# Kernel tuning notes

Hardware: AMD Instinct MI355X
Metric: run time of the kernel (lower is better)

Reference implementation:

```python
import jax, jax.numpy as jnp
import numpy as np
from jax.scipy.special import logsumexp

B, T, F = 32, 256, 32   # batch, line width (time), line height (features)
HID = 128
VOCAB = 100             # blank index = VOCAB
LBL = 32                # label length
NEG = -1e30


def _mdlstm(x, Wx, Wh1, Wh2, b):
    # x: [B, H, W, C] -> 2D LSTM: outer scan over width, inner scan over height
    Bb, H, W, C = x.shape
    hid = Wh1.shape[0]

    def col_step(carry, x_col):
        c_left, h_left = carry  # [H, B, hid] states from previous column

        def row_step(rc, inp):
            c_up, h_up = rc          # [B, hid] from previous row
            x_ij, c_l, h_l = inp     # [B, C], [B, hid], [B, hid]
            z = x_ij @ Wx + h_l @ Wh1 + h_up @ Wh2 + b  # [B, 5*hid]
            i_, g_, f1, f2, o_ = jnp.split(z, 5, axis=-1)
            c = jax.nn.sigmoid(f1) * c_l + jax.nn.sigmoid(f2) * c_up + jax.nn.sigmoid(i_) * jnp.tanh(g_)
            h = jax.nn.sigmoid(o_) * jnp.tanh(c)
            return (c, h), (c, h)

        z0 = jnp.zeros((Bb, hid), x.dtype)
        _, (c_col, h_col) = jax.lax.scan(row_step, (z0, z0), (x_col, c_left, h_left))
        return (c_col, h_col), h_col

    x_t = jnp.transpose(x, (2, 1, 0, 3))  # [W, H, B, C]
    zc = jnp.zeros((H, Bb, hid), x.dtype)
    _, hs = jax.lax.scan(col_step, (zc, zc), x_t)  # [W, H, B, hid]
    return jnp.transpose(hs, (2, 1, 0, 3))  # [B, H, W, hid]


def _ctc_loss(logp, labels, blank):
    # logp: [B, T, V] log-softmax; labels: [B, L] int in [0, blank)
    Bb, Tt, V = logp.shape
    Ll = labels.shape[1]
    S = 2 * Ll + 1
    ext = jnp.full((Bb, S), blank, dtype=labels.dtype).at[:, 1::2].set(labels)  # blank-interleaved
    lp_ext = jnp.take_along_axis(logp, jnp.broadcast_to(ext[:, None, :], (Bb, Tt, S)), axis=2)  # [B,T,S]
    prev2 = jnp.concatenate([jnp.full((Bb, 2), blank, dtype=ext.dtype), ext[:, :-2]], axis=1)
    skip = (ext != blank) & (ext != prev2)
    skip = skip.at[:, :2].set(False)
    alpha0 = jnp.full((Bb, S), NEG, logp.dtype).at[:, 0].set(lp_ext[:, 0, 0]).at[:, 1].set(lp_ext[:, 0, 1])

    def step(alpha, lp_t):
        a1 = jnp.concatenate([jnp.full((Bb, 1), NEG, alpha.dtype), alpha[:, :-1]], axis=1)
        a2 = jnp.concatenate([jnp.full((Bb, 2), NEG, alpha.dtype), alpha[:, :-2]], axis=1)
        a2 = jnp.where(skip, a2, NEG)
        new = logsumexp(jnp.stack([alpha, a1, a2], axis=0), axis=0) + lp_t
        return new, None

    alphaT, _ = jax.lax.scan(step, alpha0, jnp.transpose(lp_ext, (1, 0, 2))[1:])
    ll = logsumexp(jnp.stack([alphaT[:, -1], alphaT[:, -2]], axis=0), axis=0)
    return -ll  # [B]


def setup_inputs() -> dict:
    key = jax.random.key(0)
    ks = jax.random.split(key, 8)
    s = 0.08
    return {
        "X": jax.random.normal(ks[0], (B, T, F), jnp.float32),
        "y": jax.random.randint(ks[1], (B, LBL), 0, VOCAB),
        "Wx": jax.random.normal(ks[2], (1, 5 * HID), jnp.float32) * s,
        "Wh1": jax.random.normal(ks[3], (HID, 5 * HID), jnp.float32) * s,
        "Wh2": jax.random.normal(ks[4], (HID, 5 * HID), jnp.float32) * s,
        "b": jax.random.normal(ks[5], (5 * HID,), jnp.float32) * 0.01,
        "W_fc": jax.random.normal(ks[6], (HID, VOCAB + 1), jnp.float32) * s,
        "b_fc": jax.random.normal(ks[7], (VOCAB + 1,), jnp.float32) * 0.01,
    }


def reference(X, y, Wx, Wh1, Wh2, b, W_fc, b_fc):
    x = jnp.transpose(X, (0, 2, 1))[..., None]        # [B, F, T, 1] (image)
    h = _mdlstm(x, Wx, Wh1, Wh2, b)                    # [B, F, T, HID]
    feat = jnp.sum(h, axis=1)                          # collapse over height -> [B, T, HID]
    logits = feat @ W_fc + b_fc                        # [B, T, VOCAB+1]
    logp = jax.nn.log_softmax(logits, axis=-1)
    return _ctc_loss(logp, y, VOCAB)                   # per-example CTC loss [B]
```

## Files before the change

### kernel.cpp

```cpp
#include <hip/hip_runtime.h>

#define NEGF (-1e30f)

typedef __attribute__((ext_vector_type(8))) short short8;
typedef __attribute__((ext_vector_type(4))) float float4v;

template <bool V> struct BC { static constexpr bool value = V; };

__device__ __forceinline__ short f2bf(float f) {
  union { float f; unsigned u; } v; v.f = f;
  unsigned r = v.u + 0x7fffu + ((v.u >> 16) & 1u);
  return (short)(r >> 16);
}
__device__ __forceinline__ float fastrcp(float x) { return __builtin_amdgcn_rcpf(x); }
__device__ __forceinline__ float clamp15(float x) { return fminf(15.0f, fmaxf(-15.0f, x)); }

__global__ void prep_w_kernel(const float* __restrict__ Wh1, const float* __restrict__ Wh2,
                              short* __restrict__ wsW) {
  int t = blockIdx.x * 256 + threadIdx.x;
  int lane = t & 63;
  int frag = t >> 6;
  int nt = frag >> 3, kk = frag & 7;
  int n  = nt * 16 + (lane & 15);
  int kb = kk * 32 + (lane >> 4) * 8;
  short8 v;
#pragma unroll
  for (int j = 0; j < 8; ++j) {
    int k = kb + j;
    float w = (k < 128) ? Wh1[k * 640 + n] : Wh2[(k - 128) * 640 + n];
    v[j] = f2bf(w);
  }
  ((short8*)wsW)[frag * 64 + lane] = v;
}

__global__ __launch_bounds__(512)
void mdlstm_kernel(const float* __restrict__ X, const short* __restrict__ wsW,
                   const float* __restrict__ Wx, const float* __restrict__ bias,
                   float* __restrict__ feat, float* __restrict__ bH0,
                   float* __restrict__ bC0, int* __restrict__ flagA,
                   int* __restrict__ flagB) {
  __shared__ __align__(16) short h_buf[2][17][136];
  __shared__ __align__(16) short wlds[128 * 512];
  __shared__ __align__(16) short wlds2[16 * 512];

  const int blk  = blockIdx.x;
  const int bat  = blk >> 1;
  const bool isB = blk & 1;
  const int tid  = threadIdx.x;
  const int lane = tid & 63;
  const int g    = tid >> 6;
  const int col  = lane & 15;
  const int quad = lane >> 4;
  const int jj   = g * 16 + col;

  for (int i = tid; i < 2 * 17 * 136 / 2; i += 512) ((int*)h_buf)[i] = 0;
  {
    const uint4* src = (const uint4*)(wsW + 192 * 512);
    uint4* dst = (uint4*)wlds;
    for (int i = tid; i < 8192; i += 512) dst[i] = src[i];
    const uint4* s4 = (const uint4*)wsW;
    uint4* d2 = (uint4*)wlds2;
    for (int i = tid; i < 1024; i += 512) {
      int f = i >> 6, off = i & 63;
      int srcf = 128 + 8 * (f >> 1) + (f & 1);
      d2[i] = s4[srcf * 64 + off];
    }
  }

  float wx[5], bg[5];
#pragma unroll
  for (int q = 0; q < 5; ++q) {
    wx[q] = Wx[q * 128 + jj];
    bg[q] = bias[q * 128 + jj];
  }
  float cp[4] = {0.f, 0.f, 0.f, 0.f};
  float c15 = 0.0f;

  const float* Xg = X + bat * 8192;
  float* fb = feat + bat * 32768;
  float* bH = bH0 + bat * 32 * 128;
  float* bC = bC0 + bat * 32 * 128;
  int* fA = flagA + bat;
  int* fB = flagB + bat;
  const short8* W8 = (const short8*)wsW;
  const short8* pW0 = W8 + ((0 * 8 + g) * 8) * 64 + lane;
  const short8* pW1 = W8 + ((1 * 8 + g) * 8) * 64 + lane;
  const short8* pW2 = W8 + ((2 * 8 + g) * 8) * 64 + lane;
  const short8* pL3 = (const short8*)&wlds[((0 * 8 + g) * 8) * 512 + lane * 8];
  const short8* pL4 = (const short8*)&wlds[((1 * 8 + g) * 8) * 512 + lane * 8];
  const short8* pL2 = (const short8*)&wlds2[(g * 2) * 512 + lane * 8];
  const int mbase = (isB ? 16 : 0) + quad * 4;
  const int widx0 = (isB ? 1 : 0) + quad * 4;
  const float* pX = Xg - 31 * mbase;
  float* pF = fb + jj - 128 * mbase;
  __syncthreads();

  auto step = [&](int d, auto isb_, auto allv_) {
    constexpr bool IsB = decltype(isb_)::value;
    constexpr bool ALLV = decltype(allv_)::value;
    const int rbuf = (d + 1) & 1, wbuf = d & 1;
    float4v acc[5];
#pragma unroll
    for (int q = 0; q < 5; ++q) acc[q] = (float4v){bg[q], bg[q], bg[q], bg[q]};
    const short8 z8 = (short8){0, 0, 0, 0, 0, 0, 0, 0};
#pragma unroll
    for (int kk = 0; kk < 8; ++kk) {
      const int up = (kk >= 4) ? 1 : 0;
      const int cc = (kk & 3) * 32 + quad * 8;
      int row = col + (IsB ? 1 : 0) - up;
      short8 a0 = (IsB || row >= 0) ? *(const short8*)&h_buf[rbuf][row][cc] : z8;
      short8 b3 = pL3[kk * 64];
      acc[3] = __builtin_amdgcn_mfma_f32_16x16x32_bf16(a0, b3, acc[3], 0, 0, 0);
      short8 b4 = pL4[kk * 64];
      acc[4] = __builtin_amdgcn_mfma_f32_16x16x32_bf16(a0, b4, acc[4], 0, 0, 0);
      short8 b2 = (kk < 2) ? pL2[kk * 64] : pW2[kk * 64];
      acc[2] = __builtin_amdgcn_mfma_f32_16x16x32_bf16(a0, b2, acc[2], 0, 0, 0);
      short8 b0 = pW0[kk * 64];
      acc[0] = __builtin_amdgcn_mfma_f32_16x16x32_bf16(a0, b0, acc[0], 0, 0, 0);
      short8 b1 = pW1[kk * 64];
      acc[1] = __builtin_amdgcn_mfma_f32_16x16x32_bf16(a0, b1, acc[1], 0, 0, 0);
    }

    float t0 = __shfl_up(cp[3], 16);
    float cu[4];
    cu[0] = quad ? t0 : (IsB ? c15 : 0.0f);
    cu[1] = cp[0]; cu[2] = cp[1]; cu[3] = cp[2];
    const float* pXd = pX + d * 32;
    float* pFd = pF + d * 128;
    float xm[4];
#pragma unroll
    for (int r = 0; r < 4; ++r) {
      int w = d - (mbase + r);
      if (ALLV || (w >= 0 && w < 256)) xm[r] = pXd[-31 * r];
    }
#pragma unroll
    for (int r = 0; r < 4; ++r) {
      const int w = d - (mbase + r);
      if (ALLV || (w >= 0 && w < 256)) {
        float c_up = cu[r];
        float c_l  = cp[r];
        float x    = xm[r];
        float zi = clamp15(fmaf(x, wx[0], acc[0][r]));
        float zg = clamp15(fmaf(x, wx[1], acc[1][r]));
        float z1 = clamp15(fmaf(x, wx[2], acc[2][r]));
        float z2 = clamp15(fmaf(x, wx[3], acc[3][r]));
        float zo = clamp15(fmaf(x, wx[4], acc[4][r]));
        float e1 = __expf(z1), e2 = __expf(z2), ei = __expf(zi), eg = __expf(2.0f * zg);
        float A1 = 1.0f + e1, A2 = 1.0f + e2, Ai = 1.0f + ei, G = 1.0f + eg;
        float P = Ai * G, Q = A1 * A2;
        float rD = fastrcp(P * Q);
        float c = (e1 * c_l * (A2 * P) + e2 * c_up * (A1 * P) + ei * (eg - 1.0f) * Q) * rD;
        float eo = __expf(-zo);
        float ec = __expf(2.0f * clamp15(c));
        float h = (ec - 1.0f) * fastrcp((1.0f + eo) * (ec + 1.0f));
        cp[r] = c;
        h_buf[wbuf][widx0 + r][jj] = f2bf(h);
        atomicAdd(&pFd[-128 * r], h);
        if (!IsB && r == 3 && quad == 3 && d >= 15) {
          const int slot = (d & 31) * 128 + jj;
          atomicExch(&bH[slot], h);
          atomicExch(&bC[slot], c);
        }
      }
    }
  };

  auto receive = [&](int e) {
    if (e <= 271) {
      if (lane == 0) { while (atomicAdd(fA, 0) < e) {} }
      const int slot = ((e - 1) & 31) * 128 + jj;
      if (quad == 1) {
        float hv = atomicAdd(&bH[slot], 0.0f);
        h_buf[(e + 1) & 1][0][jj] = f2bf(hv);
      } else if (quad == 0) {
        c15 = atomicAdd(&bC[slot], 0.0f);
      }
    } else {
      if (quad == 1) h_buf[(e + 1) & 1][0][jj] = 0;
      else if (quad == 0) c15 = 0.0f;
    }
  };

  BC<true> T; BC<false> F;
  if (!isB) {
    for (int d = 0; d < 15; ++d)   { step(d, F, F); __syncthreads(); }
    for (int d = 15; d < 256; ++d) {
      if (d >= 47 && lane == 0) { while (atomicAdd(fB, 0) < d - 32) {} }
      step(d, F, T); __syncthreads();
      if (tid == 0) atomicExch(fA, d + 1);
    }
    for (int d = 256; d < 271; ++d) {
      if (lane == 0) { while (atomicAdd(fB, 0) < d - 32) {} }
      step(d, F, F); __syncthreads();
      if (tid == 0) atomicExch(fA, d + 1);
    }
  } else {
    receive(16);
    for (int d = 16; d < 31; ++d)  { __syncthreads(); step(d, T, F); receive(d + 1); if (tid == 0) atomicExch(fB, d); }
    for (int d = 31; d < 272; ++d) { __syncthreads(); step(d, T, T); receive(d + 1); if (tid == 0) atomicExch(fB, d); }
    for (int d = 272; d < 287; ++d){ __syncthreads(); step(d, T, F); if (d < 286) receive(d + 1); if (tid == 0) atomicExch(fB, d); }
  }
}

__global__ __launch_bounds__(256)
void logits_kernel(const float* __restrict__ feat, const float* __restrict__ Wfc,
                   const float* __restrict__ bfc, float* __restrict__ logp) {
  __shared__ float sW[128 * 101];
  __shared__ float sF[8][128];
  __shared__ float sL[8][104];
  __shared__ float sLse[8];
  const int tid = threadIdx.x;
  const int b  = blockIdx.x >> 5;
  const int t0 = (blockIdx.x & 31) * 8;

  for (int i = tid; i < 128 * 101; i += 256) sW[i] = Wfc[i];
  for (int i = tid; i < 8 * 128; i += 256)
    sF[i >> 7][i & 127] = feat[(b * 256 + t0 + (i >> 7)) * 128 + (i & 127)];
  __syncthreads();
  for (int idx = tid; idx < 8 * 101; idx += 256) {
    int tr = idx / 101, v = idx - tr * 101;
    float s = bfc[v];
#pragma unroll 4
    for (int k = 0; k < 128; ++k) s += sF[tr][k] * sW[k * 101 + v];
    sL[tr][v] = s;
  }
  __syncthreads();
  if (tid < 8) {
    float m = NEGF;
    for (int v = 0; v < 101; ++v) m = fmaxf(m, sL[tid][v]);
    float su = 0.0f;
    for (int v = 0; v < 101; ++v) su += __expf(sL[tid][v] - m);
    sLse[tid] = m + __logf(su);
  }
  __syncthreads();
  for (int idx = tid; idx < 8 * 101; idx += 256) {
    int tr = idx / 101, v = idx - tr * 101;
    logp[(b * 256 + t0 + tr) * 101 + v] = sL[tr][v] - sLse[tr];
  }
}

__global__ __launch_bounds__(64)
void ctc_kernel(const float* __restrict__ logp, const int* __restrict__ y,
                float* __restrict__ out) {
  const int b = blockIdx.x;
  const int l = threadIdx.x;
  const float* lpb = logp + b * 256 * 101;
  const int* yb = y + b * 32;
  int lab = (l & 1) ? yb[l >> 1] : 100;
  bool skip = (l & 1) && (l >= 3) && (yb[l >> 1] != yb[(l >> 1) - 1]);

  float a   = (l == 0) ? lpb[100] : ((l == 1) ? lpb[lab] : NEGF);
  float a64 = NEGF;
  float pl[4], pb[4];
#pragma unroll
  for (int tt = 0; tt < 4; ++tt) {
    pl[tt] = lpb[(1 + tt) * 101 + lab];
    pb[tt] = lpb[(1 + tt) * 101 + 100];
  }
#pragma unroll 4
  for (int t = 1; t < 256; ++t) {
    const int s = (t - 1) & 3;
    float lpl = pl[s], lpbk = pb[s];
    if (t + 4 < 256) {
      pl[s] = lpb[(t + 4) * 101 + lab];
      pb[s] = lpb[(t + 4) * 101 + 100];
    }
    float am1 = __shfl_up(a, 1); if (l == 0) am1 = NEGF;
    float am2 = __shfl_up(a, 2); if (l < 2 || !skip) am2 = NEGF;
    float m3 = fmaxf(a, fmaxf(am1, am2));
    float na = m3 + __logf(__expf(a - m3) + __expf(am1 - m3) + __expf(am2 - m3)) + lpl;
    float m2 = fmaxf(a64, a);
    float na64 = m2 + __logf(__expf(a64 - m2) + __expf(a - m2)) + lpbk;
    a = na;
    a64 = na64;
  }
  float A63 = __shfl(a, 63);
  float A64 = __shfl(a64, 63);
  if (l == 0) {
    float m = fmaxf(A63, A64);
    out[b] = -(m + __logf(__expf(A63 - m) + __expf(A64 - m)));
  }
}

extern "C" void kernel_launch(void* const* d_in, const int* in_sizes, int n_in,
                              void* d_out, int out_size, void* d_ws, size_t ws_size,
                              hipStream_t stream) {
  const float* X   = (const float*)d_in[0];
  const int*   y   = (const int*)d_in[1];
  const float* Wx  = (const float*)d_in[2];
  const float* Wh1 = (const float*)d_in[3];
  const float* Wh2 = (const float*)d_in[4];
  const float* bi  = (const float*)d_in[5];
  const float* Wfc = (const float*)d_in[6];
  const float* bfc = (const float*)d_in[7];
  float* out = (float*)d_out;

  char* ws = (char*)d_ws;
  short* wsW  = (short*)(ws);
  float* bndH = (float*)(ws + 0x50000);
  float* bndC = (float*)(ws + 0xD0000);
  int*   flgA = (int*)(ws + 0x150000);
  int*   flgB = (int*)(ws + 0x150800);
  float* logp = (float*)(ws + 0x50000);
  float* feat = (float*)(ws + 0x378000);

  hipMemsetAsync(feat, 0, 32 * 256 * 128 * sizeof(float), stream);
  prep_w_kernel<<<80, 256, 0, stream>>>(Wh1, Wh2, wsW);
  mdlstm_kernel<<<64, 512, 0, stream>>>(X, wsW, Wx, bi, feat, bndH, bndC, flgA, flgB);
  logits_kernel<<<1024, 256, 0, stream>>>(feat, Wfc, bfc, logp);
  ctc_kernel<<<32, 64, 0, stream>>>(logp, y, out);
}
```

Baseline: 877.2 us.

## Merge two-block split MDLSTM into one block per batch with register-held weights

Each batch element previously ran on two cooperating blocks that traded boundary h/c state through global memory with spin-wait flags. Now a single 512-thread block handles all 32 rows, running two MFMA row-halves per wavefront step and passing the row-16 cell state by warp shuffle. Gate weights for three gates sit in registers and the other two in LDS. Per-column feature sums build up in an LDS ring buffer instead of global atomics. This removes the cross-block flag handshakes and atomic traffic, but doubles per-block MFMA work each diagonal, halves the block count, and raises register pressure.

```diff
diff --git a/kernel.cpp b/kernel.cpp
--- a/kernel.cpp
+++ b/kernel.cpp
@@ -36,16 +36,12 @@
 __global__ __launch_bounds__(512)
 void mdlstm_kernel(const float* __restrict__ X, const short* __restrict__ wsW,
                    const float* __restrict__ Wx, const float* __restrict__ bias,
-                   float* __restrict__ feat, float* __restrict__ bH0,
-                   float* __restrict__ bC0, int* __restrict__ flagA,
-                   int* __restrict__ flagB) {
-  __shared__ __align__(16) short h_buf[2][17][136];
-  __shared__ __align__(16) short wlds[128 * 512];
-  __shared__ __align__(16) short wlds2[16 * 512];
-
-  const int blk  = blockIdx.x;
-  const int bat  = blk >> 1;
-  const bool isB = blk & 1;
+                   float* __restrict__ feat) {
+  __shared__ __align__(16) short h_buf[2][33][136];
+  __shared__ __align__(16) short wlds[14 * 4096];
+  __shared__ float featbuf[33][132];
+
+  const int bat  = blockIdx.x;
   const int tid  = threadIdx.x;
   const int lane = tid & 63;
   const int g    = tid >> 6;
@@ -53,17 +49,17 @@
   const int quad = lane >> 4;
   const int jj   = g * 16 + col;
 
-  for (int i = tid; i < 2 * 17 * 136 / 2; i += 512) ((int*)h_buf)[i] = 0;
+  for (int i = tid; i < 4488; i += 512) ((int*)h_buf)[i] = 0;
+  for (int i = tid; i < 33 * 132; i += 512) ((float*)featbuf)[i] = 0.0f;
   {
-    const uint4* src = (const uint4*)(wsW + 192 * 512);
-    uint4* dst = (uint4*)wlds;
-    for (int i = tid; i < 8192; i += 512) dst[i] = src[i];
     const uint4* s4 = (const uint4*)wsW;
-    uint4* d2 = (uint4*)wlds2;
-    for (int i = tid; i < 1024; i += 512) {
-      int f = i >> 6, off = i & 63;
-      int srcf = 128 + 8 * (f >> 1) + (f & 1);
-      d2[i] = s4[srcf * 64 + off];
+    uint4* d4 = (uint4*)wlds;
+    for (int i = tid; i < 14 * 512; i += 512) {
+      int c = i >> 9, off = i & 511;
+      int gg = off >> 6, ln = off & 63;
+      int q  = (c < 7) ? 3 : 4;
+      int kk = (c < 7) ? c : (c - 7);
+      d4[i] = s4[(((q * 8 + gg) * 8) + kk) * 64 + ln];
     }
   }
 
@@ -73,133 +69,115 @@
     wx[q] = Wx[q * 128 + jj];
     bg[q] = bias[q * 128 + jj];
   }
-  float cp[4] = {0.f, 0.f, 0.f, 0.f};
-  float c15 = 0.0f;
-
-  const float* Xg = X + bat * 8192;
+
+  const short8* W8 = (const short8*)wsW;
+  short8 rb0[8], rb1[8], rb2[8];
+#pragma unroll
+  for (int kk = 0; kk < 8; ++kk) {
+    rb0[kk] = W8[((0 * 8 + g) * 8 + kk) * 64 + lane];
+    rb1[kk] = W8[((1 * 8 + g) * 8 + kk) * 64 + lane];
+    rb2[kk] = W8[((2 * 8 + g) * 8 + kk) * 64 + lane];
+  }
+  const short8 rb37 = W8[((3 * 8 + g) * 8 + 7) * 64 + lane];
+  const short8 rb47 = W8[((4 * 8 + g) * 8 + 7) * 64 + lane];
+
+  const short8* pL3 = (const short8*)wlds + g * 64 + lane;
+  const short8* pL4 = (const short8*)wlds + 7 * 512 + g * 64 + lane;
+
+  float cp0[4] = {0.f, 0.f, 0.f, 0.f};
+  float cp1[4] = {0.f, 0.f, 0.f, 0.f};
+  const float* Xb = X + bat * 8192;
   float* fb = feat + bat * 32768;
-  float* bH = bH0 + bat * 32 * 128;
-  float* bC = bC0 + bat * 32 * 128;
-  int* fA = flagA + bat;
-  int* fB = flagB + bat;
-  const short8* W8 = (const short8*)wsW;
-  const short8* pW0 = W8 + ((0 * 8 + g) * 8) * 64 + lane;
-  const short8* pW1 = W8 + ((1 * 8 + g) * 8) * 64 + lane;
-  const short8* pW2 = W8 + ((2 * 8 + g) * 8) * 64 + lane;
-  const short8* pL3 = (const short8*)&wlds[((0 * 8 + g) * 8) * 512 + lane * 8];
-  const short8* pL4 = (const short8*)&wlds[((1 * 8 + g) * 8) * 512 + lane * 8];
-  const short8* pL2 = (const short8*)&wlds2[(g * 2) * 512 + lane * 8];
-  const int mbase = (isB ? 16 : 0) + quad * 4;
-  const int widx0 = (isB ? 1 : 0) + quad * 4;
-  const float* pX = Xg - 31 * mbase;
-  float* pF = fb + jj - 128 * mbase;
-  __syncthreads();
-
-  auto step = [&](int d, auto isb_, auto allv_) {
-    constexpr bool IsB = decltype(isb_)::value;
+
+  int sb = 0;
+  __syncthreads();
+
+  auto stepT = [&](int d, auto allv_) {
     constexpr bool ALLV = decltype(allv_)::value;
     const int rbuf = (d + 1) & 1, wbuf = d & 1;
-    float4v acc[5];
-#pragma unroll
-    for (int q = 0; q < 5; ++q) acc[q] = (float4v){bg[q], bg[q], bg[q], bg[q]};
-    const short8 z8 = (short8){0, 0, 0, 0, 0, 0, 0, 0};
+
+    if (d >= 32 && tid < 128) {
+      int fs = sb + 1; if (fs >= 33) fs = 0;
+      float v = featbuf[fs][tid];
+      featbuf[fs][tid] = 0.0f;
+      fb[(d - 32) * 128 + tid] = v;
+    }
+
+    float4v acc0[5], acc1[5];
+#pragma unroll
+    for (int q = 0; q < 5; ++q) {
+      acc0[q] = (float4v){bg[q], bg[q], bg[q], bg[q]};
+      acc1[q] = acc0[q];
+    }
 #pragma unroll
     for (int kk = 0; kk < 8; ++kk) {
-      const int up = (kk >= 4) ? 1 : 0;
-      const int cc = (kk & 3) * 32 + quad * 8;
-      int row = col + (IsB ? 1 : 0) - up;
-      short8 a0 = (IsB || row >= 0) ? *(const short8*)&h_buf[rbuf][row][cc] : z8;
-      short8 b3 = pL3[kk * 64];
-      acc[3] = __builtin_amdgcn_mfma_f32_16x16x32_bf16(a0, b3, acc[3], 0, 0, 0);
-      short8 b4 = pL4[kk * 64];
-      acc[4] = __builtin_amdgcn_mfma_f32_16x16x32_bf16(a0, b4, acc[4], 0, 0, 0);
-      short8 b2 = (kk < 2) ? pL2[kk * 64] : pW2[kk * 64];
-      acc[2] = __builtin_amdgcn_mfma_f32_16x16x32_bf16(a0, b2, acc[2], 0, 0, 0);
-      short8 b0 = pW0[kk * 64];
-      acc[0] = __builtin_amdgcn_mfma_f32_16x16x32_bf16(a0, b0, acc[0], 0, 0, 0);
-      short8 b1 = pW1[kk * 64];
-      acc[1] = __builtin_amdgcn_mfma_f32_16x16x32_bf16(a0, b1, acc[1], 0, 0, 0);
-    }
-
-    float t0 = __shfl_up(cp[3], 16);
-    float cu[4];
-    cu[0] = quad ? t0 : (IsB ? c15 : 0.0f);
-    cu[1] = cp[0]; cu[2] = cp[1]; cu[3] = cp[2];
-    const float* pXd = pX + d * 32;
-    float* pFd = pF + d * 128;
-    float xm[4];
-#pragma unroll
-    for (int r = 0; r < 4; ++r) {
-      int w = d - (mbase + r);
-      if (ALLV || (w >= 0 && w < 256)) xm[r] = pXd[-31 * r];
-    }
-#pragma unroll
-    for (int r = 0; r < 4; ++r) {
-      const int w = d - (mbase + r);
-      if (ALLV || (w >= 0 && w < 256)) {
-        float c_up = cu[r];
-        float c_l  = cp[r];
-        float x    = xm[r];
-        float zi = clamp15(fmaf(x, wx[0], acc[0][r]));
-        float zg = clamp15(fmaf(x, wx[1], acc[1][r]));
-        float z1 = clamp15(fmaf(x, wx[2], acc[2][r]));
-        float z2 = clamp15(fmaf(x, wx[3], acc[3][r]));
-        float zo = clamp15(fmaf(x, wx[4], acc[4][r]));
-        float e1 = __expf(z1), e2 = __expf(z2), ei = __expf(zi), eg = __expf(2.0f * zg);
-        float A1 = 1.0f + e1, A2 = 1.0f + e2, Ai = 1.0f + ei, G = 1.0f + eg;
-        float P = Ai * G, Q = A1 * A2;
-        float rD = fastrcp(P * Q);
-        float c = (e1 * c_l * (A2 * P) + e2 * c_up * (A1 * P) + ei * (eg - 1.0f) * Q) * rD;
-        float eo = __expf(-zo);
-        float ec = __expf(2.0f * clamp15(c));
-        float h = (ec - 1.0f) * fastrcp((1.0f + eo) * (ec + 1.0f));
-        cp[r] = c;
-        h_buf[wbuf][widx0 + r][jj] = f2bf(h);
-        atomicAdd(&pFd[-128 * r], h);
-        if (!IsB && r == 3 && quad == 3 && d >= 15) {
-          const int slot = (d & 31) * 128 + jj;
-          atomicExch(&bH[slot], h);
-          atomicExch(&bC[slot], c);
+      const int up = kk >> 2;
+      const int ccc = (kk & 3) * 32 + quad * 8;
+      short8 a0 = *(const short8*)&h_buf[rbuf][col + 1 - up][ccc];
+      short8 a1 = *(const short8*)&h_buf[rbuf][17 + col - up][ccc];
+      short8 b3 = (kk < 7) ? pL3[kk * 512] : rb37;
+      acc0[3] = __builtin_amdgcn_mfma_f32_16x16x32_bf16(a0, b3, acc0[3], 0, 0, 0);
+      acc1[3] = __builtin_amdgcn_mfma_f32_16x16x32_bf16(a1, b3, acc1[3], 0, 0, 0);
+      short8 b4 = (kk < 7) ? pL4[kk * 512] : rb47;
+      acc0[4] = __builtin_amdgcn_mfma_f32_16x16x32_bf16(a0, b4, acc0[4], 0, 0, 0);
+      acc1[4] = __builtin_amdgcn_mfma_f32_16x16x32_bf16(a1, b4, acc1[4], 0, 0, 0);
+      short8 b0 = rb0[kk];
+      acc0[0] = __builtin_amdgcn_mfma_f32_16x16x32_bf16(a0, b0, acc0[0], 0, 0, 0);
+      acc1[0] = __builtin_amdgcn_mfma_f32_16x16x32_bf16(a1, b0, acc1[0], 0, 0, 0);
+      short8 b1 = rb1[kk];
+      acc0[1] = __builtin_amdgcn_mfma_f32_16x16x32_bf16(a0, b1, acc0[1], 0, 0, 0);
+      acc1[1] = __builtin_amdgcn_mfma_f32_16x16x32_bf16(a1, b1, acc1[1], 0, 0, 0);
+      short8 b2 = rb2[kk];
+      acc0[2] = __builtin_amdgcn_mfma_f32_16x16x32_bf16(a0, b2, acc0[2], 0, 0, 0);
+      acc1[2] = __builtin_amdgcn_mfma_f32_16x16x32_bf16(a1, b2, acc1[2], 0, 0, 0);
+    }
+
+    float t00 = __shfl_up(cp0[3], 16);
+    float t10 = __shfl_up(cp1[3], 16);
+    float c15 = __shfl(cp0[3], 48 + col);
+    float cu0[4], cu1[4];
+    cu0[0] = quad ? t00 : 0.0f; cu0[1] = cp0[0]; cu0[2] = cp0[1]; cu0[3] = cp0[2];
+    cu1[0] = quad ? t10 : c15;  cu1[1] = cp1[0]; cu1[2] = cp1[1]; cu1[3] = cp1[2];
+
+    auto halfc = [&](float4v (&acc)[5], float (&cp)[4], float (&cu)[4], int mbase) {
+#pragma unroll
+      for (int r = 0; r < 4; ++r) {
+        const int m = mbase + r;
+        const int w = d - m;
+        if (ALLV || (unsigned)w < 256u) {
+          const float x = Xb[w * 32 + m];
+          float zi = clamp15(fmaf(x, wx[0], acc[0][r]));
+          float zg = clamp15(fmaf(x, wx[1], acc[1][r]));
+          float z1 = clamp15(fmaf(x, wx[2], acc[2][r]));
+          float z2 = clamp15(fmaf(x, wx[3], acc[3][r]));
+          float zo = clamp15(fmaf(x, wx[4], acc[4][r]));
+          float e1 = __expf(z1), e2 = __expf(z2), ei = __expf(zi), eg = __expf(2.0f * zg);
+          float A1 = 1.0f + e1, A2 = 1.0f + e2, Ai = 1.0f + ei, G = 1.0f + eg;
+          float P = Ai * G, Q = A1 * A2;
+          float rD = fastrcp(P * Q);
+          float c = (e1 * cp[r] * (A2 * P) + e2 * cu[r] * (A1 * P) + ei * (eg - 1.0f) * Q) * rD;
+          float eo = __expf(-zo);
+          float ec = __expf(2.0f * clamp15(c));
+          float h = (ec - 1.0f) * fastrcp((1.0f + eo) * (ec + 1.0f));
+          cp[r] = c;
+          h_buf[wbuf][1 + m][jj] = f2bf(h);
+          int s = sb - m; if (s < 0) s += 33;
+          featbuf[s][jj] += h;
         }
       }
-    }
+    };
+    halfc(acc0, cp0, cu0, quad * 4);
+    halfc(acc1, cp1, cu1, 16 + quad * 4);
+    __syncthreads();
   };
 
-  auto receive = [&](int e) {
-    if (e <= 271) {
-      if (lane == 0) { while (atomicAdd(fA, 0) < e) {} }
-      const int slot = ((e - 1) & 31) * 128 + jj;
-      if (quad == 1) {
-        float hv = atomicAdd(&bH[slot], 0.0f);
-        h_buf[(e + 1) & 1][0][jj] = f2bf(hv);
-      } else if (quad == 0) {
-        c15 = atomicAdd(&bC[slot], 0.0f);
-      }
-    } else {
-      if (quad == 1) h_buf[(e + 1) & 1][0][jj] = 0;
-      else if (quad == 0) c15 = 0.0f;
-    }
-  };
-
-  BC<true> T; BC<false> F;
-  if (!isB) {
-    for (int d = 0; d < 15; ++d)   { step(d, F, F); __syncthreads(); }
-    for (int d = 15; d < 256; ++d) {
-      if (d >= 47 && lane == 0) { while (atomicAdd(fB, 0) < d - 32) {} }
-      step(d, F, T); __syncthreads();
-      if (tid == 0) atomicExch(fA, d + 1);
-    }
-    for (int d = 256; d < 271; ++d) {
-      if (lane == 0) { while (atomicAdd(fB, 0) < d - 32) {} }
-      step(d, F, F); __syncthreads();
-      if (tid == 0) atomicExch(fA, d + 1);
-    }
-  } else {
-    receive(16);
-    for (int d = 16; d < 31; ++d)  { __syncthreads(); step(d, T, F); receive(d + 1); if (tid == 0) atomicExch(fB, d); }
-    for (int d = 31; d < 272; ++d) { __syncthreads(); step(d, T, T); receive(d + 1); if (tid == 0) atomicExch(fB, d); }
-    for (int d = 272; d < 287; ++d){ __syncthreads(); step(d, T, F); if (d < 286) receive(d + 1); if (tid == 0) atomicExch(fB, d); }
-  }
+  BC<true> Tv; BC<false> Fv;
+  for (int d = 0; d < 31; ++d)    { stepT(d, Fv); sb = (sb == 32) ? 0 : sb + 1; }
+  for (int d = 31; d < 256; ++d)  { stepT(d, Tv); sb = (sb == 32) ? 0 : sb + 1; }
+  for (int d = 256; d < 287; ++d) { stepT(d, Fv); sb = (sb == 32) ? 0 : sb + 1; }
+
+  int fs = sb + 1; if (fs >= 33) fs = 0;
+  if (tid < 128) fb[255 * 128 + tid] = featbuf[fs][tid];
 }
 
 __global__ __launch_bounds__(256)
@@ -297,16 +275,12 @@
 
   char* ws = (char*)d_ws;
   short* wsW  = (short*)(ws);
-  float* bndH = (float*)(ws + 0x50000);
-  float* bndC = (float*)(ws + 0xD0000);
-  int*   flgA = (int*)(ws + 0x150000);
-  int*   flgB = (int*)(ws + 0x150800);
   float* logp = (float*)(ws + 0x50000);
   float* feat = (float*)(ws + 0x378000);
 
   hipMemsetAsync(feat, 0, 32 * 256 * 128 * sizeof(float), stream);
   prep_w_kernel<<<80, 256, 0, stream>>>(Wh1, Wh2, wsW);
-  mdlstm_kernel<<<64, 512, 0, stream>>>(X, wsW, Wx, bi, feat, bndH, bndC, flgA, flgB);
+  mdlstm_kernel<<<32, 512, 0, stream>>>(X, wsW, Wx, bi, feat);
   logits_kernel<<<1024, 256, 0, stream>>>(feat, Wfc, bfc, logp);
   ctc_kernel<<<32, 64, 0, stream>>>(logp, y, out);
 }
```

Result: slower. 1.080 ms (+23.1%).

## Batch cross-block flag handoffs and accumulate features in LDS ring buffer

Applied to the files above, without the earlier changes.

Replaces the per-diagonal global atomicAdd of every h value into feat with an LDS ring buffer (featbuf) that sums rows over the height dimension and flushes one column per step with 128 atomics. The inter-block handshake between the two halves now signals and polls flags only every 8 diagonals, and the B half prefetches the boundary h/c values one step ahead, cutting spin-wait and sync latency on the serial wavefront. It also drops the wlds2 weight cache so LDS can hold the feature buffer, which moves part of the Wh2 fragment loads back to global memory. It also adds more lag and more ring buffer-slot bookkeeping that must stay consistent.

```diff
diff --git a/kernel.cpp b/kernel.cpp
--- a/kernel.cpp
+++ b/kernel.cpp
@@ -41,7 +41,7 @@
                    int* __restrict__ flagB) {
   __shared__ __align__(16) short h_buf[2][17][136];
   __shared__ __align__(16) short wlds[128 * 512];
-  __shared__ __align__(16) short wlds2[16 * 512];
+  __shared__ float featbuf[17][132];
 
   const int blk  = blockIdx.x;
   const int bat  = blk >> 1;
@@ -54,17 +54,11 @@
   const int jj   = g * 16 + col;
 
   for (int i = tid; i < 2 * 17 * 136 / 2; i += 512) ((int*)h_buf)[i] = 0;
+  for (int i = tid; i < 17 * 132; i += 512) ((float*)featbuf)[i] = 0.0f;
   {
     const uint4* src = (const uint4*)(wsW + 192 * 512);
     uint4* dst = (uint4*)wlds;
     for (int i = tid; i < 8192; i += 512) dst[i] = src[i];
-    const uint4* s4 = (const uint4*)wsW;
-    uint4* d2 = (uint4*)wlds2;
-    for (int i = tid; i < 1024; i += 512) {
-      int f = i >> 6, off = i & 63;
-      int srcf = 128 + 8 * (f >> 1) + (f & 1);
-      d2[i] = s4[srcf * 64 + off];
-    }
   }
 
   float wx[5], bg[5];
@@ -75,6 +69,8 @@
   }
   float cp[4] = {0.f, 0.f, 0.f, 0.f};
   float c15 = 0.0f;
+  float pre_h = 0.0f, pre_c = 0.0f;
+  int knownA = 0;
 
   const float* Xg = X + bat * 8192;
   float* fb = feat + bat * 32768;
@@ -88,17 +84,25 @@
   const short8* pW2 = W8 + ((2 * 8 + g) * 8) * 64 + lane;
   const short8* pL3 = (const short8*)&wlds[((0 * 8 + g) * 8) * 512 + lane * 8];
   const short8* pL4 = (const short8*)&wlds[((1 * 8 + g) * 8) * 512 + lane * 8];
-  const short8* pL2 = (const short8*)&wlds2[(g * 2) * 512 + lane * 8];
   const int mbase = (isB ? 16 : 0) + quad * 4;
   const int widx0 = (isB ? 1 : 0) + quad * 4;
   const float* pX = Xg - 31 * mbase;
-  float* pF = fb + jj - 128 * mbase;
+  int sb = 0;
   __syncthreads();
 
   auto step = [&](int d, auto isb_, auto allv_) {
     constexpr bool IsB = decltype(isb_)::value;
     constexpr bool ALLV = decltype(allv_)::value;
     const int rbuf = (d + 1) & 1, wbuf = d & 1;
+
+    const int wfl = d - (IsB ? 32 : 16);
+    if (wfl >= 0 && tid < 128) {
+      int fs = sb + 1; if (fs >= 17) fs = 0;
+      float v = featbuf[fs][tid];
+      featbuf[fs][tid] = 0.0f;
+      atomicAdd(&fb[wfl * 128 + tid], v);
+    }
+
     float4v acc[5];
 #pragma unroll
     for (int q = 0; q < 5; ++q) acc[q] = (float4v){bg[q], bg[q], bg[q], bg[q]};
@@ -113,7 +117,7 @@
       acc[3] = __builtin_amdgcn_mfma_f32_16x16x32_bf16(a0, b3, acc[3], 0, 0, 0);
       short8 b4 = pL4[kk * 64];
       acc[4] = __builtin_amdgcn_mfma_f32_16x16x32_bf16(a0, b4, acc[4], 0, 0, 0);
-      short8 b2 = (kk < 2) ? pL2[kk * 64] : pW2[kk * 64];
+      short8 b2 = pW2[kk * 64];
       acc[2] = __builtin_amdgcn_mfma_f32_16x16x32_bf16(a0, b2, acc[2], 0, 0, 0);
       short8 b0 = pW0[kk * 64];
       acc[0] = __builtin_amdgcn_mfma_f32_16x16x32_bf16(a0, b0, acc[0], 0, 0, 0);
@@ -126,7 +130,6 @@
     cu[0] = quad ? t0 : (IsB ? c15 : 0.0f);
     cu[1] = cp[0]; cu[2] = cp[1]; cu[3] = cp[2];
     const float* pXd = pX + d * 32;
-    float* pFd = pF + d * 128;
     float xm[4];
 #pragma unroll
     for (int r = 0; r < 4; ++r) {
@@ -155,7 +158,8 @@
         float h = (ec - 1.0f) * fastrcp((1.0f + eo) * (ec + 1.0f));
         cp[r] = c;
         h_buf[wbuf][widx0 + r][jj] = f2bf(h);
-        atomicAdd(&pFd[-128 * r], h);
+        int s = sb - (quad * 4 + r); if (s < 0) s += 17;
+        featbuf[s][jj] += h;
         if (!IsB && r == 3 && quad == 3 && d >= 15) {
           const int slot = (d & 31) * 128 + jj;
           atomicExch(&bH[slot], h);
@@ -165,40 +169,54 @@
     }
   };
 
-  auto receive = [&](int e) {
-    if (e <= 271) {
-      if (lane == 0) { while (atomicAdd(fA, 0) < e) {} }
-      const int slot = ((e - 1) & 31) * 128 + jj;
-      if (quad == 1) {
-        float hv = atomicAdd(&bH[slot], 0.0f);
-        h_buf[(e + 1) & 1][0][jj] = f2bf(hv);
-      } else if (quad == 0) {
-        c15 = atomicAdd(&bC[slot], 0.0f);
+  BC<true> Tv; BC<false> Fv;
+  if (!isB) {
+    auto aiter = [&](int d, auto allv) {
+      if (d >= 48 && (d & 7) == 0 && lane == 0) {
+        while (atomicAdd(fB, 0) < d - 22) {}
       }
-    } else {
-      if (quad == 1) h_buf[(e + 1) & 1][0][jj] = 0;
-      else if (quad == 0) c15 = 0.0f;
-    }
-  };
-
-  BC<true> T; BC<false> F;
-  if (!isB) {
-    for (int d = 0; d < 15; ++d)   { step(d, F, F); __syncthreads(); }
-    for (int d = 15; d < 256; ++d) {
-      if (d >= 47 && lane == 0) { while (atomicAdd(fB, 0) < d - 32) {} }
-      step(d, F, T); __syncthreads();
-      if (tid == 0) atomicExch(fA, d + 1);
-    }
-    for (int d = 256; d < 271; ++d) {
-      if (lane == 0) { while (atomicAdd(fB, 0) < d - 32) {} }
-      step(d, F, F); __syncthreads();
-      if (tid == 0) atomicExch(fA, d + 1);
-    }
+      step(d, Fv, allv);
+      sb = (sb == 16) ? 0 : sb + 1;
+      __syncthreads();
+      if ((((d + 1) & 7) == 0 || d == 270) && tid == 0) atomicExch(fA, d + 1);
+    };
+    for (int d = 0; d < 15; ++d)    aiter(d, Fv);
+    for (int d = 15; d < 256; ++d)  aiter(d, Tv);
+    for (int d = 256; d < 271; ++d) aiter(d, Fv);
+    if (tid < 128) atomicAdd(&fb[255 * 128 + tid], featbuf[0][tid]);
   } else {
-    receive(16);
-    for (int d = 16; d < 31; ++d)  { __syncthreads(); step(d, T, F); receive(d + 1); if (tid == 0) atomicExch(fB, d); }
-    for (int d = 31; d < 272; ++d) { __syncthreads(); step(d, T, T); receive(d + 1); if (tid == 0) atomicExch(fB, d); }
-    for (int d = 272; d < 287; ++d){ __syncthreads(); step(d, T, F); if (d < 286) receive(d + 1); if (tid == 0) atomicExch(fB, d); }
+    {
+      if (lane == 0) { while (atomicAdd(fA, 0) < 23) {} knownA = 23; }
+      const int slot = 15 * 128 + jj;
+      if (quad == 1) pre_h = atomicAdd(&bH[slot], 0.0f);
+      else if (quad == 0) pre_c = atomicAdd(&bC[slot], 0.0f);
+    }
+    auto biter = [&](int e, auto allv) {
+      if (quad == 1) h_buf[(e + 1) & 1][0][jj] = f2bf(pre_h);
+      else if (quad == 0) c15 = pre_c;
+      const int ee = e + 1;
+      if (ee <= 271) {
+        if (lane == 0 && knownA < ee) {
+          int tgt = ee + 7; if (tgt > 271) tgt = 271;
+          while (atomicAdd(fA, 0) < tgt) {}
+          knownA = tgt;
+        }
+        const int slot = ((ee - 1) & 31) * 128 + jj;
+        if (quad == 1) pre_h = atomicAdd(&bH[slot], 0.0f);
+        else if (quad == 0) pre_c = atomicAdd(&bC[slot], 0.0f);
+      } else {
+        pre_h = 0.0f; pre_c = 0.0f;
+      }
+      __syncthreads();
+      step(e, Tv, allv);
+      sb = (sb == 16) ? 0 : sb + 1;
+      if (((e & 7) == 7 || e == 286) && tid == 0) atomicExch(fB, e);
+    };
+    for (int e = 16; e < 31; ++e)   biter(e, Fv);
+    for (int e = 31; e < 272; ++e)  biter(e, Tv);
+    for (int e = 272; e < 287; ++e) biter(e, Fv);
+    __syncthreads();
+    if (tid < 128) atomicAdd(&fb[255 * 128 + tid], featbuf[0][tid]);
   }
 }
 
```

After: 866.3 us. No clear change (-1.2%).
